# Kernel tuning notes

Hardware: AMD Instinct MI355X
Metric: run time of the kernel (lower is better)

The kernel has to match this reference:

```python
import jax, jax.numpy as jnp
import numpy as np

NUM_BUSES = 20000
NUM_LINES = 320000
OTHER = 1000
BATCH = 128


def setup_inputs() -> dict:
    key = jax.random.key(0)
    k1, k2, k3, k4, k5 = jax.random.split(key, 5)
    x = jax.random.normal(k1, (BATCH, 2 * NUM_BUSES + OTHER), dtype=jnp.float32)
    from_indices = jax.random.randint(k2, (NUM_LINES,), 0, NUM_BUSES, dtype=jnp.int32)
    to_indices = jax.random.randint(k3, (NUM_LINES,), 0, NUM_BUSES, dtype=jnp.int32)
    # reactances bounded away from 0 (realistic p.u. line reactances)
    reactances = 0.01 + 0.2 * jax.random.uniform(k4, (NUM_LINES,), dtype=jnp.float32)
    limits = 0.5 + 1.5 * jax.random.uniform(k5, (NUM_LINES,), dtype=jnp.float32)
    return {
        "x": x,
        "from_indices": from_indices,
        "to_indices": to_indices,
        "reactances": reactances,
        "limits": limits,
        "num_buses": NUM_BUSES,
    }


def reference(x, from_indices, to_indices, reactances, limits, num_buses):
    nb = num_buses
    voltages = x[:, :nb]                     # [B, nb]
    angles = x[:, nb:2 * nb]                 # [B, nb]
    other_params = x[:, 2 * nb:]             # [B, other]

    from_a = angles[:, from_indices]         # [B, L] gather
    to_a = angles[:, to_indices]
    angle_diffs = from_a - to_a
    flows = angle_diffs / reactances[None, :]
    over = jnp.abs(flows / limits[None, :]) > 1.0

    # Torch runs this branch only if any line is over limit; when none are,
    # adjustments are identically zero, so applying unconditionally is exact.
    required = jnp.sign(angle_diffs) * (reactances * limits)[None, :]
    adjustments = jnp.where(over, required, angle_diffs) - angle_diffs  # [B, L]
    half = adjustments * 0.5
    # angles = angles + from_adjustments - to_adjustments
    #        = angles + scatter_add(from, adj/2) + scatter_add(to, adj/2)
    # (torch accumulates -adj/2 into to_adjustments, then subtracts it)
    delta = jnp.zeros_like(angles).at[:, from_indices].add(half).at[:, to_indices].add(half)
    angles2 = angles + delta

    diffs2 = angles2[:, from_indices] - angles2[:, to_indices]
    flows2 = diffs2 / reactances[None, :]

    out = jnp.concatenate([voltages, angles2, other_params], axis=1)
    return out, flows2
```

## Files before the change

kernel.cpp:

```cpp
#include <hip/hip_runtime.h>

#define NB     20000
#define NL     320000
#define NOTH   1000
#define BATCH  128
#define ROW    (2*NB + NOTH)
#define CAP    80
#define BCHUNK 8
#define CB     (NB/BCHUNK)
#define NSLICE 2
#define LPS    (NL/NSLICE)

__device__ __forceinline__ float fast_rcp(float a)
{
    float r;
    asm volatile("v_rcp_f32 %0, %1" : "=v"(r) : "v"(a));
    return r;
}

__global__ __launch_bounds__(256) void build_k(
    const int* __restrict__ fidx, const int* __restrict__ tidx,
    const float* __restrict__ xr, const float* __restrict__ lim,
    int* __restrict__ cnt, unsigned* __restrict__ bins)
{
    const int l = blockIdx.x * 256 + threadIdx.x;
    if (l >= NL) return;
    const int fi = fidx[l];
    const int ti = tidx[l];
    union { float f; unsigned u; } c; c.f = xr[l] * lim[l];
    const unsigned rl16 = (c.u + 0x8000u) >> 16;

    const unsigned wf = ((unsigned)ti << 17) | rl16;
    const unsigned wt = ((unsigned)fi << 17) | (1u << 16) | rl16;

    const int p0 = atomicAdd(&cnt[fi], 1);
    if (p0 < CAP) bins[(size_t)p0 * NB + fi] = wf;
    const int p1 = atomicAdd(&cnt[ti], 1);
    if (p1 < CAP) bins[(size_t)p1 * NB + ti] = wt;
}

__global__ __launch_bounds__(256) void copy_k(
    const float* __restrict__ x, float* __restrict__ out)
{
    const int i = blockIdx.x * 256 + threadIdx.x;
    const int q = ROW / 4;
    if (i >= BATCH * q) return;
    const int e = (i % q) * 4;
    if (e >= NB && e < 2 * NB) return;
    ((float4*)out)[i] = ((const float4*)x)[i];
}

__device__ __forceinline__ float contrib(unsigned w, float ab, const float* a)
{
    const int   other = (int)(w >> 17);
    const float rl    = __uint_as_float((w & 0xFFFFu) << 16);
    const float ad    = ab - a[other];
    float h = 0.0f;
    if (fabsf(ad) > rl) {
        h = 0.5f * (copysignf(rl, ad) - ad);
        if (w & (1u << 16)) h = -h;
    }
    return h;
}

__global__ __launch_bounds__(1024) void delta_k(
    const float* __restrict__ x, const int* __restrict__ cnt,
    const unsigned* __restrict__ bins, float* __restrict__ out)
{
    extern __shared__ float a[];
    const int b  = blockIdx.x % BATCH;
    const int cb = blockIdx.x / BATCH;

    const float* __restrict__ ang = x + (size_t)b * ROW + NB;
    for (int i = threadIdx.x; i < NB / 4; i += 1024)
        ((float4*)a)[i] = ((const float4*)ang)[i];
    __syncthreads();

    float* __restrict__ orow = out + (size_t)b * ROW + NB;
    const int base = cb * CB;
    for (int bus = base + (int)threadIdx.x; bus < base + CB; bus += 1024) {
        const int   n  = min(cnt[bus], CAP);
        const float ab = a[bus];
        float ds = 0.0f;
        int k = 0;
        for (; k + 4 <= n; k += 4) {
            const unsigned w0 = bins[(size_t)(k + 0) * NB + bus];
            const unsigned w1 = bins[(size_t)(k + 1) * NB + bus];
            const unsigned w2 = bins[(size_t)(k + 2) * NB + bus];
            const unsigned w3 = bins[(size_t)(k + 3) * NB + bus];
            ds += contrib(w0, ab, a) + contrib(w1, ab, a)
                + contrib(w2, ab, a) + contrib(w3, ab, a);
        }
        for (; k < n; ++k)
            ds += contrib(bins[(size_t)k * NB + bus], ab, a);
        orow[bus] = ab + ds;
    }
}

__global__ __launch_bounds__(1024) void flows_lds_k(
    const float* __restrict__ out, const int* __restrict__ fidx,
    const int* __restrict__ tidx, const float* __restrict__ xr,
    float* __restrict__ f2)
{
    extern __shared__ float a2[];
    const int b = blockIdx.x % BATCH;
    const int s = blockIdx.x / BATCH;

    const float* __restrict__ src = out + (size_t)b * ROW + NB;
    for (int i = threadIdx.x; i < NB / 4; i += 1024)
        ((float4*)a2)[i] = ((const float4*)src)[i];
    __syncthreads();

    float* __restrict__ frow = f2 + (size_t)b * NL;
    const int q0 = s * (LPS / 4);
    const int q1 = q0 + (LPS / 4);
    for (int q = q0 + (int)threadIdx.x; q < q1; q += 1024) {
        const int4   f = ((const int4*)fidx)[q];
        const int4   t = ((const int4*)tidx)[q];
        const float4 r = ((const float4*)xr)[q];
        float4 o;
        o.x = (a2[f.x] - a2[t.x]) * fast_rcp(r.x);
        o.y = (a2[f.y] - a2[t.y]) * fast_rcp(r.y);
        o.z = (a2[f.z] - a2[t.z]) * fast_rcp(r.z);
        o.w = (a2[f.w] - a2[t.w]) * fast_rcp(r.w);
        ((float4*)frow)[q] = o;
    }
}

extern "C" void kernel_launch(void* const* d_in, const int* in_sizes, int n_in,
                              void* d_out, int out_size, void* d_ws, size_t ws_size,
                              hipStream_t stream)
{
    const float* x   = (const float*)d_in[0];
    const int*   fi  = (const int*)  d_in[1];
    const int*   ti  = (const int*)  d_in[2];
    const float* xr  = (const float*)d_in[3];
    const float* lim = (const float*)d_in[4];

    float* out    = (float*)d_out;
    float* flows2 = out + (size_t)BATCH * ROW;

    int*      cnt  = (int*)d_ws;
    unsigned* bins = (unsigned*)((char*)d_ws + NB * 4);

    hipMemsetAsync(cnt, 0, NB * sizeof(int), stream);

    build_k<<<dim3((NL + 255) / 256), dim3(256), 0, stream>>>(
        fi, ti, xr, lim, cnt, bins);

    copy_k<<<dim3((BATCH * (ROW / 4) + 255) / 256), dim3(256), 0, stream>>>(
        x, out);

    delta_k<<<dim3(BCHUNK * BATCH), dim3(1024), NB * 4, stream>>>(
        x, cnt, bins, out);

    flows_lds_k<<<dim3(NSLICE * BATCH), dim3(1024), NB * 4, stream>>>(
        out, fi, ti, xr, flows2);
}
```

Before: 130.8 us.

## Fuse passthrough copy into delta kernel, vectorize bin build, replace memset

Removes the standalone copy kernel: each delta block now copies its chunk of voltages, and block chunk 0 also copies the other parameters. The build kernel handles four lines per thread with vector loads, and the memset is replaced by a small zeroing kernel. The aim is fewer launches and less per-thread overhead in the atomic binning, at the cost of more work per delta block and less atomic parallelism per thread.

```diff
diff --git a/kernel.cpp b/kernel.cpp
--- a/kernel.cpp
+++ b/kernel.cpp
@@ -18,36 +18,40 @@
     return r;
 }
 
+__global__ __launch_bounds__(256) void zero_k(int* __restrict__ cnt)
+{
+    const int i = blockIdx.x * 256 + threadIdx.x;
+    if (i < NB / 4) ((int4*)cnt)[i] = make_int4(0, 0, 0, 0);
+}
+
 __global__ __launch_bounds__(256) void build_k(
     const int* __restrict__ fidx, const int* __restrict__ tidx,
     const float* __restrict__ xr, const float* __restrict__ lim,
     int* __restrict__ cnt, unsigned* __restrict__ bins)
 {
-    const int l = blockIdx.x * 256 + threadIdx.x;
-    if (l >= NL) return;
-    const int fi = fidx[l];
-    const int ti = tidx[l];
-    union { float f; unsigned u; } c; c.f = xr[l] * lim[l];
-    const unsigned rl16 = (c.u + 0x8000u) >> 16;
+    const int q = blockIdx.x * 256 + threadIdx.x;
+    if (q >= NL / 4) return;
+    const int4   f = ((const int4*)fidx)[q];
+    const int4   t = ((const int4*)tidx)[q];
+    const float4 r = ((const float4*)xr)[q];
+    const float4 L = ((const float4*)lim)[q];
 
-    const unsigned wf = ((unsigned)ti << 17) | rl16;
-    const unsigned wt = ((unsigned)fi << 17) | (1u << 16) | rl16;
-
-    const int p0 = atomicAdd(&cnt[fi], 1);
-    if (p0 < CAP) bins[(size_t)p0 * NB + fi] = wf;
-    const int p1 = atomicAdd(&cnt[ti], 1);
-    if (p1 < CAP) bins[(size_t)p1 * NB + ti] = wt;
-}
-
-__global__ __launch_bounds__(256) void copy_k(
-    const float* __restrict__ x, float* __restrict__ out)
-{
-    const int i = blockIdx.x * 256 + threadIdx.x;
-    const int q = ROW / 4;
-    if (i >= BATCH * q) return;
-    const int e = (i % q) * 4;
-    if (e >= NB && e < 2 * NB) return;
-    ((float4*)out)[i] = ((const float4*)x)[i];
+    #define EMIT(FI, TI, RC, LC)                                             \
+    {                                                                        \
+        union { float f; unsigned u; } c; c.f = (RC) * (LC);                 \
+        const unsigned rl16 = (c.u + 0x8000u) >> 16;                         \
+        const int p0 = atomicAdd(&cnt[FI], 1);                               \
+        if (p0 < CAP) bins[(size_t)p0 * NB + (FI)] =                         \
+            ((unsigned)(TI) << 17) | rl16;                                   \
+        const int p1 = atomicAdd(&cnt[TI], 1);                               \
+        if (p1 < CAP) bins[(size_t)p1 * NB + (TI)] =                         \
+            ((unsigned)(FI) << 17) | (1u << 16) | rl16;                      \
+    }
+    EMIT(f.x, t.x, r.x, L.x)
+    EMIT(f.y, t.y, r.y, L.y)
+    EMIT(f.z, t.z, r.z, L.z)
+    EMIT(f.w, t.w, r.w, L.w)
+    #undef EMIT
 }
 
 __device__ __forceinline__ float contrib(unsigned w, float ab, const float* a)
@@ -63,7 +67,7 @@
     return h;
 }
 
-__global__ __launch_bounds__(1024) void delta_k(
+__global__ __launch_bounds__(1024) void delta_copy_k(
     const float* __restrict__ x, const int* __restrict__ cnt,
     const unsigned* __restrict__ bins, float* __restrict__ out)
 {
@@ -71,12 +75,19 @@
     const int b  = blockIdx.x % BATCH;
     const int cb = blockIdx.x / BATCH;
 
-    const float* __restrict__ ang = x + (size_t)b * ROW + NB;
+    const float* __restrict__ xrow = x   + (size_t)b * ROW;
+    float*       __restrict__ orow = out + (size_t)b * ROW;
+
     for (int i = threadIdx.x; i < NB / 4; i += 1024)
-        ((float4*)a)[i] = ((const float4*)ang)[i];
+        ((float4*)a)[i] = ((const float4*)(xrow + NB))[i];
     __syncthreads();
 
-    float* __restrict__ orow = out + (size_t)b * ROW + NB;
+    for (int i = threadIdx.x; i < CB / 4; i += 1024)
+        ((float4*)(orow + cb * CB))[i] = ((const float4*)(xrow + cb * CB))[i];
+    if (cb == 0)
+        for (int i = threadIdx.x; i < NOTH / 4; i += 1024)
+            ((float4*)(orow + 2 * NB))[i] = ((const float4*)(xrow + 2 * NB))[i];
+
     const int base = cb * CB;
     for (int bus = base + (int)threadIdx.x; bus < base + CB; bus += 1024) {
         const int   n  = min(cnt[bus], CAP);
@@ -93,7 +104,7 @@
         }
         for (; k < n; ++k)
             ds += contrib(bins[(size_t)k * NB + bus], ab, a);
-        orow[bus] = ab + ds;
+        orow[NB + bus] = ab + ds;
     }
 }
 
@@ -143,15 +154,12 @@
     int*      cnt  = (int*)d_ws;
     unsigned* bins = (unsigned*)((char*)d_ws + NB * 4);
 
-    hipMemsetAsync(cnt, 0, NB * sizeof(int), stream);
+    zero_k<<<dim3((NB / 4 + 255) / 256), dim3(256), 0, stream>>>(cnt);
 
-    build_k<<<dim3((NL + 255) / 256), dim3(256), 0, stream>>>(
+    build_k<<<dim3((NL / 4 + 255) / 256), dim3(256), 0, stream>>>(
         fi, ti, xr, lim, cnt, bins);
 
-    copy_k<<<dim3((BATCH * (ROW / 4) + 255) / 256), dim3(256), 0, stream>>>(
-        x, out);
-
-    delta_k<<<dim3(BCHUNK * BATCH), dim3(1024), NB * 4, stream>>>(
+    delta_copy_k<<<dim3(BCHUNK * BATCH), dim3(1024), NB * 4, stream>>>(
         x, cnt, bins, out);
 
     flows_lds_k<<<dim3(NSLICE * BATCH), dim3(1024), NB * 4, stream>>>(
```

After: 128.2 us. Within noise of the previous version (-2.0%).
